# Kernel optimization log

Measured on AMD Instinct MI355X. Metric: run time of the kernel, lower is better.

The kernel has to match this reference:

```python
import math
import jax, jax.numpy as jnp
import numpy as np


def conv2d(x, w, b, pad=0, dil=1):
    # x: [B, Cin, H, W], w: [Cout, Cin, kh, kw] (OIHW)
    y = jax.lax.conv_general_dilated(
        x, w, window_strides=(1, 1),
        padding=[(pad, pad), (pad, pad)],
        rhs_dilation=(dil, dil),
        dimension_numbers=('NCHW', 'OIHW', 'NCHW'))
    return y + b[None, :, None, None]


def setup_inputs() -> dict:
    key = jax.random.key(0)
    ks = jax.random.split(key, 8)
    B, C, H, W = 2, 64, 96, 96
    inner = 64 // 18  # = 3, as in the torch module
    n_dil = 3
    s = 0.1
    x = jax.random.normal(ks[0], (B, C, H, W), jnp.float32)
    w_red = jax.random.normal(ks[1], (inner, C, 1, 1), jnp.float32) * s
    b_red = jax.random.normal(ks[2], (inner,), jnp.float32) * s
    w_dil = jax.random.normal(ks[3], (n_dil, inner, inner, 3, 3), jnp.float32) * s
    b_dil = jax.random.normal(ks[4], (n_dil, inner), jnp.float32) * s
    w_fuse = jax.random.normal(ks[5], (C, inner * n_dil * 6, 1, 1), jnp.float32) * s
    b_fuse = jax.random.normal(ks[6], (C,), jnp.float32) * s
    return {"x": x, "w_red": w_red, "b_red": b_red, "w_dil": w_dil,
            "b_dil": b_dil, "w_fuse": w_fuse, "b_fuse": b_fuse}


def _c4_transforms(x):
    # identity, flip-W, flip-H, rot90 k=1,2,3 over spatial dims
    return [x,
            jnp.flip(x, axis=-1),
            jnp.flip(x, axis=-2),
            jnp.rot90(x, 1, axes=(2, 3)),
            jnp.rot90(x, 2, axes=(2, 3)),
            jnp.rot90(x, 3, axes=(2, 3))]


def reference(x, w_red, b_red, w_dil, b_dil, w_fuse, b_fuse):
    dilations = (1, 2, 3)
    residual_scale = 0.2
    B, C, H, W = x.shape
    x_red = conv2d(x, w_red, b_red)                    # [B, inner, H, W]
    tfs = _c4_transforms(x_red)
    feats = []
    for i, d in enumerate(dilations):
        co = conv2d(x_red, w_dil[i], b_dil[i], pad=d, dil=d)
        for tf in tfs:
            feats.append(co * tf)
    cat = jnp.concatenate(feats, axis=1)               # [B, inner*18, H, W]
    fused = conv2d(cat, w_fuse, b_fuse)                # [B, C, H, W]
    tokens = fused.reshape(B, C, H * W).transpose(0, 2, 1)  # [B, N, C]
    # Chunked attention in the original is mathematically full self-attention
    scores = jnp.einsum('bnc,bmc->bnm', tokens, tokens) / math.sqrt(C)
    attn = jax.nn.softmax(scores, axis=-1)
    out = jnp.einsum('bnm,bmc->bnc', attn, tokens)     # [B, N, C]
    out = out.transpose(0, 2, 1).reshape(B, C, H, W)
    return x + residual_scale * out
```

## Files before the change

kernel.cpp:

```cpp
#include <hip/hip_runtime.h>

#define HW    96
#define NPIX  9216
#define NCH   64
#define INNER 3
#define NDIL  3
#define BB    2
#define TOTPIX (BB * NPIX)
#define NT32  (NPIX / 32)

typedef __attribute__((ext_vector_type(8))) short short8;
typedef __attribute__((ext_vector_type(8))) unsigned short ushort8;
typedef __attribute__((ext_vector_type(4))) float f32x4;
typedef __attribute__((ext_vector_type(4))) unsigned int uint32x4;

__device__ __forceinline__ ushort f2bf_rne(float f) {
    unsigned u = __float_as_uint(f);
    u += 0x7fffu + ((u >> 16) & 1u);
    return (ushort)(u >> 16);
}
__device__ __forceinline__ float bf2f(ushort u) {
    return __uint_as_float((unsigned)u << 16);
}
__device__ __forceinline__ unsigned pack_bf(float lo, float hi) {
    return __builtin_amdgcn_perm(__float_as_uint(hi), __float_as_uint(lo), 0x07060302u);
}

__global__ __launch_bounds__(256) void
k_reduce(const float* __restrict__ x, const float* __restrict__ w_red,
         const float* __restrict__ b_red, float* __restrict__ xred,
         float* __restrict__ L) {
    __shared__ float part[4][3][64];
    int tid = threadIdx.x;
    int gid = blockIdx.x * 256 + tid;
    if (gid < TOTPIX) L[gid] = 0.f;
    int cp = tid >> 6, lane = tid & 63;
    int pix = blockIdx.x * 64 + lane;
    int b = pix / NPIX, n = pix % NPIX;
    const float* xb = x + (size_t)b * NCH * NPIX + (size_t)(cp * 16) * NPIX + n;
    float a0 = 0.f, a1 = 0.f, a2 = 0.f;
    #pragma unroll
    for (int c = 0; c < 16; ++c) {
        float xv = xb[(size_t)c * NPIX];
        a0 = fmaf(w_red[0 * NCH + cp * 16 + c], xv, a0);
        a1 = fmaf(w_red[1 * NCH + cp * 16 + c], xv, a1);
        a2 = fmaf(w_red[2 * NCH + cp * 16 + c], xv, a2);
    }
    part[cp][0][lane] = a0; part[cp][1][lane] = a1; part[cp][2][lane] = a2;
    __syncthreads();
    if (tid < 192) {
        int o = tid >> 6, lp = tid & 63;
        float s = ((part[0][o][lp] + part[1][o][lp]) +
                   (part[2][o][lp] + part[3][o][lp])) + b_red[o];
        int pix2 = blockIdx.x * 64 + lp;
        int b2 = pix2 / NPIX, n2 = pix2 % NPIX;
        xred[((size_t)b2 * INNER + o) * NPIX + n2] = s;
    }
}

__global__ __launch_bounds__(256) void
k_featfuse(const float* __restrict__ xred, const float* __restrict__ w_dil,
           const float* __restrict__ b_dil, const float* __restrict__ w_fuse,
           const float* __restrict__ b_fuse, ushort* __restrict__ tok,
           ushort* __restrict__ tokTt) {
    __shared__ ushort wpad[64 * 72];
    __shared__ float  bsh[64];
    __shared__ ushort FTt[64 * 70];
    __shared__ ushort tile[64 * 72];

    int tid = threadIdx.x;
    for (int i = tid; i < 64 * 64; i += 256) {
        int c = i >> 6, j = i & 63;
        wpad[c * 72 + j] = (j < 54) ? f2bf_rne(w_fuse[c * 54 + j]) : (ushort)0;
    }
    if (tid < 64) bsh[tid] = b_fuse[tid];

    int px0 = blockIdx.x * 64;

    if (tid < 192) {
        int lp = tid & 63, i3 = tid >> 6;
        int pix = px0 + lp;
        int b = pix / NPIX, n = pix % NPIX;
        int h = n / HW, w = n % HW;
        const float* xr = xred + (size_t)b * INNER * NPIX;
        int d = i3 + 1;

        float co[3] = {b_dil[i3 * 3 + 0], b_dil[i3 * 3 + 1], b_dil[i3 * 3 + 2]};
        #pragma unroll
        for (int ci = 0; ci < 3; ++ci) {
            const float* xo = xr + ci * NPIX;
            #pragma unroll
            for (int kh = 0; kh < 3; ++kh) {
                int hh = h + (kh - 1) * d;
                #pragma unroll
                for (int kw = 0; kw < 3; ++kw) {
                    int ww = w + (kw - 1) * d;
                    float v = ((unsigned)hh < HW && (unsigned)ww < HW)
                                  ? xo[hh * HW + ww] : 0.f;
                    #pragma unroll
                    for (int o = 0; o < 3; ++o)
                        co[o] = fmaf(w_dil[(9 * i3 + 3 * o + ci) * 9 + kh * 3 + kw],
                                     v, co[o]);
                }
            }
        }

        float tf[6][3];
        #pragma unroll
        for (int o = 0; o < 3; ++o) {
            const float* xo = xr + o * NPIX;
            tf[0][o] = xo[h * HW + w];
            tf[1][o] = xo[h * HW + (HW - 1 - w)];
            tf[2][o] = xo[(HW - 1 - h) * HW + w];
            tf[3][o] = xo[w * HW + (HW - 1 - h)];
            tf[4][o] = xo[(HW - 1 - h) * HW + (HW - 1 - w)];
            tf[5][o] = xo[(HW - 1 - w) * HW + h];
        }

        #pragma unroll
        for (int t = 0; t < 6; ++t)
            #pragma unroll
            for (int o = 0; o < 3; ++o)
                FTt[(i3 * 18 + t * 3 + o) * 70 + lp] = f2bf_rne(co[o] * tf[t][o]);
    } else {
        for (int i = tid - 192; i < 640; i += 64)
            FTt[(54 + (i >> 6)) * 70 + (i & 63)] = (ushort)0;
    }
    __syncthreads();

    int wv = tid >> 6, lane = tid & 63, quad = lane >> 4, l15 = lane & 15;

    short8 af[4][2];
    #pragma unroll
    for (int m = 0; m < 4; ++m)
        #pragma unroll
        for (int kc = 0; kc < 2; ++kc)
            af[m][kc] = *(const short8*)&wpad[(16 * m + l15) * 72 + quad * 8 + 32 * kc];

    f32x4 acc[4];
    #pragma unroll
    for (int m = 0; m < 4; ++m) acc[m] = (f32x4){0.f, 0.f, 0.f, 0.f};

    int pxl = wv * 16 + l15;
    #pragma unroll
    for (int kc = 0; kc < 2; ++kc) {
        short8 bf;
        #pragma unroll
        for (int jj = 0; jj < 8; ++jj)
            bf[jj] = (short)FTt[(quad * 8 + jj + 32 * kc) * 70 + pxl];
        #pragma unroll
        for (int m = 0; m < 4; ++m)
            acc[m] = __builtin_amdgcn_mfma_f32_16x16x32_bf16(af[m][kc], bf, acc[m], 0, 0, 0);
    }

    #pragma unroll
    for (int m = 0; m < 4; ++m)
        #pragma unroll
        for (int r = 0; r < 4; ++r) {
            int c = 16 * m + quad * 4 + r;
            tile[c * 72 + wv * 16 + l15] = f2bf_rne(acc[m][r] + bsh[c]);
        }
    __syncthreads();

    int b0 = px0 / NPIX, n0 = px0 % NPIX;
    {
        int lp = tid >> 2, part = tid & 3;
        ushort row[16];
        #pragma unroll
        for (int k = 0; k < 16; ++k) row[k] = tile[(part * 16 + k) * 72 + lp];
        ushort* dst = tok + ((size_t)b0 * NPIX + n0 + lp) * NCH + part * 16;
        *(ushort8*)&dst[0] = *(const ushort8*)&row[0];
        *(ushort8*)&dst[8] = *(const ushort8*)&row[8];
    }
    {
        int c = tid >> 2, seg = tid & 3;
        int n = n0 + seg * 16;
        size_t base = (((size_t)b0 * NT32 + (n >> 5)) * 64 + c) * 32 + (n & 31);
        *(ushort8*)&tokTt[base]     = *(const ushort8*)&tile[c * 72 + seg * 16];
        *(ushort8*)&tokTt[base + 8] = *(const ushort8*)&tile[c * 72 + seg * 16 + 8];
    }
}

__global__ __launch_bounds__(256, 5) void
k_attn(const ushort* __restrict__ tok, const ushort* __restrict__ tokTt,
       float* __restrict__ L, ushort* __restrict__ pacc, int P, int KP) {
    __shared__ ushort smem[9728];
    ushort* ldsK = smem;
    ushort* ldsV = smem + 4608;

    const int QW = NPIX / 128;
    int bid0 = blockIdx.x;
    int nwg = gridDim.x;
    int bid = (bid0 & 7) * (nwg >> 3) + (bid0 >> 3);
    int qc = bid % QW; int rest = bid / QW;
    int p = rest % P;  int b = rest / P;
    int tid = threadIdx.x;
    int wv = tid >> 6, lane = tid & 63;
    int quad = lane >> 4, l15 = lane & 15;

    const ushort* tb  = tok + (size_t)b * NPIX * NCH;
    const ushort* tvb = tokTt + (size_t)b * NT32 * (64 * 32);
    int qwave = qc * 128 + wv * 32;

    int sk_off = (tid >> 3) * 72 + (tid & 7) * 8;
    int svj = tid & 3;
    int sv_b0 = (tid >> 2) * 40 + 8 * ((2 * svj) & 3) + 4 * (svj >> 1);
    int sv_b1 = (tid >> 2) * 40 + 8 * ((2 * svj + 1) & 3) + 4 * (svj >> 1);

    short8 qf[2][2];
    const float scale = 0.125f * 1.44269504088896340736f;
    #pragma unroll
    for (int n = 0; n < 2; ++n) {
        const ushort* qr = tb + (size_t)(qwave + 16 * n + l15) * NCH + quad * 8;
        #pragma unroll
        for (int kc = 0; kc < 2; ++kc) {
            ushort8 raw = *(const ushort8*)(qr + 32 * kc);
            short8 f;
            #pragma unroll
            for (int e = 0; e < 8; ++e) f[e] = (short)f2bf_rne(bf2f(raw[e]) * scale);
            qf[n][kc] = f;
        }
    }

    f32x4 O[4][2];
    #pragma unroll
    for (int m = 0; m < 4; ++m)
        #pragma unroll
        for (int n = 0; n < 2; ++n) O[m][n] = (f32x4){0.f, 0.f, 0.f, 0.f};
    float lrun[2] = {0.f, 0.f};

    const float FM = 16.0f;
    const f32x4 FMc = (f32x4){-FM, -FM, -FM, -FM};

    int k0 = p * KP;
    int nt = KP / 32;

    const ushort* pK = tb + (size_t)k0 * NCH + tid * 8;
    const ushort* pV = tvb + ((size_t)(k0 >> 5)) * 2048 + tid * 8;

    {
        ushort8 gK = *(const ushort8*)pK;
        ushort8 gV = *(const ushort8*)pV;
        *(ushort8*)&ldsK[sk_off] = gK;
        uint32x4 v4 = *(uint32x4*)&gV;
        *(uint2*)&ldsV[sv_b0] = make_uint2(v4.x, v4.y);
        *(uint2*)&ldsV[sv_b1] = make_uint2(v4.z, v4.w);
    }
    __syncthreads();

    for (int t = 0; t < nt; ++t) {
        int curK = (t & 1) * 2304, curV = (t & 1) * 2560;
        bool pre = (t + 1 < nt);
        pK += 32 * NCH;  pV += 2048;

        ushort8 nK, nV;
        if (pre) {
            nK = *(const ushort8*)pK;
            nV = *(const ushort8*)pV;
        }

        short8 kd[4];
        #pragma unroll
        for (int m2 = 0; m2 < 2; ++m2)
            #pragma unroll
            for (int kc = 0; kc < 2; ++kc)
                kd[2 * m2 + kc] = *(const short8*)&ldsK[curK + (16 * m2 + l15) * 72 +
                                                       quad * 8 + 32 * kc];

        uint32x4 wac[2];
        #pragma unroll
        for (int m2 = 0; m2 < 2; ++m2) {
            f32x4 Sm[2];
            __builtin_amdgcn_s_setprio(1);
            #pragma unroll
            for (int n = 0; n < 2; ++n) {
                Sm[n] = __builtin_amdgcn_mfma_f32_16x16x32_bf16(kd[2 * m2 + 0],
                                                                qf[n][0], FMc, 0, 0, 0);
                Sm[n] = __builtin_amdgcn_mfma_f32_16x16x32_bf16(kd[2 * m2 + 1],
                                                                qf[n][1], Sm[n], 0, 0, 0);
            }
            __builtin_amdgcn_s_setprio(0);
            #pragma unroll
            for (int n = 0; n < 2; ++n) {
                float e0 = __builtin_amdgcn_exp2f(Sm[n][0]);
                float e1 = __builtin_amdgcn_exp2f(Sm[n][1]);
                float e2 = __builtin_amdgcn_exp2f(Sm[n][2]);
                float e3 = __builtin_amdgcn_exp2f(Sm[n][3]);
                lrun[n] += (e0 + e1) + (e2 + e3);
                if (m2 == 0) {
                    wac[n].x = pack_bf(e0, e1); wac[n].y = pack_bf(e2, e3);
                } else {
                    wac[n].z = pack_bf(e0, e1); wac[n].w = pack_bf(e2, e3);
                }
            }
        }

        if (pre) {
            *(ushort8*)&ldsK[(curK ^ 2304) + sk_off] = nK;
            uint32x4 v4 = *(uint32x4*)&nV;
            *(uint2*)&ldsV[(curV ^ 2560) + sv_b0] = make_uint2(v4.x, v4.y);
            *(uint2*)&ldsV[(curV ^ 2560) + sv_b1] = make_uint2(v4.z, v4.w);
        }

        short8 vf[4];
        #pragma unroll
        for (int mc = 0; mc < 4; ++mc)
            vf[mc] = *(const short8*)&ldsV[curV + (16 * mc + l15) * 40 + quad * 8];

        __builtin_amdgcn_s_setprio(1);
        #pragma unroll
        for (int n = 0; n < 2; ++n) {
            short8 bfr = *(short8*)&wac[n];
            #pragma unroll
            for (int mc = 0; mc < 4; ++mc)
                O[mc][n] = __builtin_amdgcn_mfma_f32_16x16x32_bf16(vf[mc], bfr,
                                                                   O[mc][n], 0, 0, 0);
        }
        __builtin_amdgcn_s_setprio(0);

        __syncthreads();
    }

    #pragma unroll
    for (int n = 0; n < 2; ++n) {
        lrun[n] += __shfl_xor(lrun[n], 16, 64);
        lrun[n] += __shfl_xor(lrun[n], 32, 64);
    }
    if (quad == 0) {
        #pragma unroll
        for (int n = 0; n < 2; ++n)
            atomicAdd(&L[(size_t)b * NPIX + qwave + 16 * n + l15], lrun[n]);
    }

    #pragma unroll
    for (int n = 0; n < 2; ++n) {
        int ql = wv * 32 + 16 * n + l15;
        #pragma unroll
        for (int m = 0; m < 4; ++m)
            #pragma unroll
            for (int r = 0; r < 4; ++r)
                smem[(16 * m + quad * 4 + r) * 136 + ql] = f2bf_rne(O[m][n][r]);
    }
    __syncthreads();
    size_t bp = (size_t)b * P + p;
    #pragma unroll
    for (int i = 0; i < 4; ++i) {
        int lin = i * 2048 + tid * 8;
        int c = lin >> 7, q = lin & 127;
        *(ushort8*)(pacc + (bp * NCH + c) * NPIX + qc * 128 + q) =
            *(const ushort8*)&smem[c * 136 + q];
    }
}

__global__ void k_combine(const float* __restrict__ x, const float* __restrict__ L,
                          const ushort* __restrict__ pacc, float* __restrict__ out,
                          int P) {
    int gid = blockIdx.x * blockDim.x + threadIdx.x;
    if (gid >= BB * NCH * (NPIX / 8)) return;
    int seg = gid % (NPIX / 8);
    int bc  = gid / (NPIX / 8);
    int b = bc / NCH;
    int n0 = seg * 8;
    float o[8] = {0.f, 0.f, 0.f, 0.f, 0.f, 0.f, 0.f, 0.f};
    for (int p = 0; p < P; ++p) {
        ushort8 t = *(const ushort8*)(pacc +
            (((size_t)b * P + p) * NCH + (bc % NCH)) * NPIX + n0);
        #pragma unroll
        for (int e = 0; e < 8; ++e) o[e] += bf2f(t[e]);
    }
    const float* lv = L + (size_t)b * NPIX + n0;
    const float* xb = x + (size_t)bc * NPIX + n0;
    float* ob = out + (size_t)bc * NPIX + n0;
    #pragma unroll
    for (int e = 0; e < 8; ++e)
        ob[e] = fmaf(0.2f / lv[e], o[e], xb[e]);
}

extern "C" void kernel_launch(void* const* d_in, const int* in_sizes, int n_in,
                              void* d_out, int out_size, void* d_ws, size_t ws_size,
                              hipStream_t stream) {
    const float* x      = (const float*)d_in[0];
    const float* w_red  = (const float*)d_in[1];
    const float* b_red  = (const float*)d_in[2];
    const float* w_dil  = (const float*)d_in[3];
    const float* b_dil  = (const float*)d_in[4];
    const float* w_fuse = (const float*)d_in[5];
    const float* b_fuse = (const float*)d_in[6];
    float* out = (float*)d_out;

    const size_t XRED_N = (size_t)BB * INNER * NPIX;
    const size_t TOK_N  = (size_t)BB * NPIX * NCH;
    const size_t HEAD_B = XRED_N * 4 + 2 * TOK_N * 2 + TOTPIX * 4;
    int P = 0;
    const int cands[4] = {8, 4, 2, 1};
    for (int ci = 0; ci < 4; ++ci) {
        int cp = cands[ci];
        size_t need = HEAD_B + (size_t)BB * cp * NPIX * NCH * 2;
        if (ws_size >= need) { P = cp; break; }
    }
    if (P == 0) return;

    float*  xred  = (float*)d_ws;
    ushort* tok   = (ushort*)(xred + XRED_N);
    ushort* tokTt = tok + TOK_N;
    float*  L     = (float*)(tokTt + TOK_N);
    ushort* pacc  = (ushort*)(L + TOTPIX);

    k_reduce  <<<TOTPIX / 64, 256, 0, stream>>>(x, w_red, b_red, xred, L);
    k_featfuse<<<TOTPIX / 64, 256, 0, stream>>>(xred, w_dil, b_dil, w_fuse,
                                                b_fuse, tok, tokTt);
    k_attn    <<<BB * P * (NPIX / 128), 256, 0, stream>>>(tok, tokTt, L, pacc,
                                                          P, NPIX / P);
    k_combine <<<(BB * NCH * (NPIX / 8) + 255) / 256, 256, 0, stream>>>(x, L, pacc,
                                                                        out, P);
}
```

Measured before the change: 137.8 us.

## Process two key tiles per barrier with doubled LDS double-buffering in attention

The attention loop now stages two 32-key K/V tiles per iteration into a double-buffered LDS region twice the size of before. It issues the global prefetches for both next tiles up front and runs the tile body twice between barriers, so the number of __syncthreads drops by half. The larger shared memory footprint lowers the occupancy hint from 5 to 4 blocks per CU, and more prefetch registers are live at once. It also assumes KP/32 is even.

```diff
diff --git a/kernel.cpp b/kernel.cpp
--- a/kernel.cpp
+++ b/kernel.cpp
@@ -181,12 +181,67 @@
     }
 }
 
-__global__ __launch_bounds__(256, 5) void
+__device__ __forceinline__ void
+attn_body(const ushort* __restrict__ Kb, const ushort* __restrict__ Vb,
+          int l15, int quad, const short8 (&qf)[2][2], f32x4 FMc,
+          f32x4 (&O)[4][2], float (&lrun)[2]) {
+    short8 kd[4];
+    #pragma unroll
+    for (int m2 = 0; m2 < 2; ++m2)
+        #pragma unroll
+        for (int kc = 0; kc < 2; ++kc)
+            kd[2 * m2 + kc] = *(const short8*)&Kb[(16 * m2 + l15) * 72 +
+                                                  quad * 8 + 32 * kc];
+
+    uint32x4 wac[2];
+    #pragma unroll
+    for (int m2 = 0; m2 < 2; ++m2) {
+        f32x4 Sm[2];
+        __builtin_amdgcn_s_setprio(1);
+        #pragma unroll
+        for (int n = 0; n < 2; ++n) {
+            Sm[n] = __builtin_amdgcn_mfma_f32_16x16x32_bf16(kd[2 * m2 + 0],
+                                                            qf[n][0], FMc, 0, 0, 0);
+            Sm[n] = __builtin_amdgcn_mfma_f32_16x16x32_bf16(kd[2 * m2 + 1],
+                                                            qf[n][1], Sm[n], 0, 0, 0);
+        }
+        __builtin_amdgcn_s_setprio(0);
+        #pragma unroll
+        for (int n = 0; n < 2; ++n) {
+            float e0 = __builtin_amdgcn_exp2f(Sm[n][0]);
+            float e1 = __builtin_amdgcn_exp2f(Sm[n][1]);
+            float e2 = __builtin_amdgcn_exp2f(Sm[n][2]);
+            float e3 = __builtin_amdgcn_exp2f(Sm[n][3]);
+            lrun[n] += (e0 + e1) + (e2 + e3);
+            if (m2 == 0) {
+                wac[n].x = pack_bf(e0, e1); wac[n].y = pack_bf(e2, e3);
+            } else {
+                wac[n].z = pack_bf(e0, e1); wac[n].w = pack_bf(e2, e3);
+            }
+        }
+    }
+
+    short8 vf[4];
+    #pragma unroll
+    for (int mc = 0; mc < 4; ++mc)
+        vf[mc] = *(const short8*)&Vb[(16 * mc + l15) * 40 + quad * 8];
+
+    __builtin_amdgcn_s_setprio(1);
+    #pragma unroll
+    for (int n = 0; n < 2; ++n) {
+        short8 bfr = *(short8*)&wac[n];
+        #pragma unroll
+        for (int mc = 0; mc < 4; ++mc)
+            O[mc][n] = __builtin_amdgcn_mfma_f32_16x16x32_bf16(vf[mc], bfr,
+                                                               O[mc][n], 0, 0, 0);
+    }
+    __builtin_amdgcn_s_setprio(0);
+}
+
+__global__ __launch_bounds__(256, 4) void
 k_attn(const ushort* __restrict__ tok, const ushort* __restrict__ tokTt,
        float* __restrict__ L, ushort* __restrict__ pacc, int P, int KP) {
-    __shared__ ushort smem[9728];
-    ushort* ldsK = smem;
-    ushort* ldsV = smem + 4608;
+    __shared__ ushort smem[19456];
 
     const int QW = NPIX / 128;
     int bid0 = blockIdx.x;
@@ -233,90 +288,58 @@
     const f32x4 FMc = (f32x4){-FM, -FM, -FM, -FM};
 
     int k0 = p * KP;
-    int nt = KP / 32;
+    int nw = (KP / 32) >> 1;
 
     const ushort* pK = tb + (size_t)k0 * NCH + tid * 8;
     const ushort* pV = tvb + ((size_t)(k0 >> 5)) * 2048 + tid * 8;
 
     {
-        ushort8 gK = *(const ushort8*)pK;
-        ushort8 gV = *(const ushort8*)pV;
-        *(ushort8*)&ldsK[sk_off] = gK;
-        uint32x4 v4 = *(uint32x4*)&gV;
-        *(uint2*)&ldsV[sv_b0] = make_uint2(v4.x, v4.y);
-        *(uint2*)&ldsV[sv_b1] = make_uint2(v4.z, v4.w);
-    }
+        ushort8 gK0 = *(const ushort8*)pK;
+        ushort8 gK1 = *(const ushort8*)(pK + 32 * NCH);
+        ushort8 gV0 = *(const ushort8*)pV;
+        ushort8 gV1 = *(const ushort8*)(pV + 2048);
+        *(ushort8*)&smem[sk_off] = gK0;
+        *(ushort8*)&smem[2304 + sk_off] = gK1;
+        uint32x4 v4 = *(uint32x4*)&gV0;
+        *(uint2*)&smem[4608 + sv_b0] = make_uint2(v4.x, v4.y);
+        *(uint2*)&smem[4608 + sv_b1] = make_uint2(v4.z, v4.w);
+        v4 = *(uint32x4*)&gV1;
+        *(uint2*)&smem[7168 + sv_b0] = make_uint2(v4.x, v4.y);
+        *(uint2*)&smem[7168 + sv_b1] = make_uint2(v4.z, v4.w);
+    }
+    pK += 64 * NCH;  pV += 4096;
     __syncthreads();
 
-    for (int t = 0; t < nt; ++t) {
-        int curK = (t & 1) * 2304, curV = (t & 1) * 2560;
-        bool pre = (t + 1 < nt);
-        pK += 32 * NCH;  pV += 2048;
-
-        ushort8 nK, nV;
+    for (int w = 0; w < nw; ++w) {
+        int base  = (w & 1) * 9728;
+        int obase = base ^ 9728;
+        bool pre = (w + 1 < nw);
+
+        ushort8 nK0, nK1, nV0, nV1;
         if (pre) {
-            nK = *(const ushort8*)pK;
-            nV = *(const ushort8*)pV;
-        }
-
-        short8 kd[4];
-        #pragma unroll
-        for (int m2 = 0; m2 < 2; ++m2)
-            #pragma unroll
-            for (int kc = 0; kc < 2; ++kc)
-                kd[2 * m2 + kc] = *(const short8*)&ldsK[curK + (16 * m2 + l15) * 72 +
-                                                       quad * 8 + 32 * kc];
-
-        uint32x4 wac[2];
-        #pragma unroll
-        for (int m2 = 0; m2 < 2; ++m2) {
-            f32x4 Sm[2];
-            __builtin_amdgcn_s_setprio(1);
-            #pragma unroll
-            for (int n = 0; n < 2; ++n) {
-                Sm[n] = __builtin_amdgcn_mfma_f32_16x16x32_bf16(kd[2 * m2 + 0],
-                                                                qf[n][0], FMc, 0, 0, 0);
-                Sm[n] = __builtin_amdgcn_mfma_f32_16x16x32_bf16(kd[2 * m2 + 1],
-                                                                qf[n][1], Sm[n], 0, 0, 0);
-            }
-            __builtin_amdgcn_s_setprio(0);
-            #pragma unroll
-            for (int n = 0; n < 2; ++n) {
-                float e0 = __builtin_amdgcn_exp2f(Sm[n][0]);
-                float e1 = __builtin_amdgcn_exp2f(Sm[n][1]);
-                float e2 = __builtin_amdgcn_exp2f(Sm[n][2]);
-                float e3 = __builtin_amdgcn_exp2f(Sm[n][3]);
-                lrun[n] += (e0 + e1) + (e2 + e3);
-                if (m2 == 0) {
-                    wac[n].x = pack_bf(e0, e1); wac[n].y = pack_bf(e2, e3);
-                } else {
-                    wac[n].z = pack_bf(e0, e1); wac[n].w = pack_bf(e2, e3);
-                }
-            }
-        }
-
+            nK0 = *(const ushort8*)pK;
+            nV0 = *(const ushort8*)pV;
+            nK1 = *(const ushort8*)(pK + 32 * NCH);
+            nV1 = *(const ushort8*)(pV + 2048);
+            pK += 64 * NCH;  pV += 4096;
+        }
+
+        attn_body(&smem[base], &smem[base + 4608], l15, quad, qf, FMc, O, lrun);
         if (pre) {
-            *(ushort8*)&ldsK[(curK ^ 2304) + sk_off] = nK;
-            uint32x4 v4 = *(uint32x4*)&nV;
-            *(uint2*)&ldsV[(curV ^ 2560) + sv_b0] = make_uint2(v4.x, v4.y);
-            *(uint2*)&ldsV[(curV ^ 2560) + sv_b1] = make_uint2(v4.z, v4.w);
-        }
-
-        short8 vf[4];
-        #pragma unroll
-        for (int mc = 0; mc < 4; ++mc)
-            vf[mc] = *(const short8*)&ldsV[curV + (16 * mc + l15) * 40 + quad * 8];
-
-        __builtin_amdgcn_s_setprio(1);
-        #pragma unroll
-        for (int n = 0; n < 2; ++n) {
-            short8 bfr = *(short8*)&wac[n];
-            #pragma unroll
-            for (int mc = 0; mc < 4; ++mc)
-                O[mc][n] = __builtin_amdgcn_mfma_f32_16x16x32_bf16(vf[mc], bfr,
-                                                                   O[mc][n], 0, 0, 0);
-        }
-        __builtin_amdgcn_s_setprio(0);
+            *(ushort8*)&smem[obase + sk_off] = nK0;
+            uint32x4 v4 = *(uint32x4*)&nV0;
+            *(uint2*)&smem[obase + 4608 + sv_b0] = make_uint2(v4.x, v4.y);
+            *(uint2*)&smem[obase + 4608 + sv_b1] = make_uint2(v4.z, v4.w);
+        }
+
+        attn_body(&smem[base + 2304], &smem[base + 7168], l15, quad, qf, FMc,
+                  O, lrun);
+        if (pre) {
+            *(ushort8*)&smem[obase + 2304 + sk_off] = nK1;
+            uint32x4 v4 = *(uint32x4*)&nV1;
+            *(uint2*)&smem[obase + 7168 + sv_b0] = make_uint2(v4.x, v4.y);
+            *(uint2*)&smem[obase + 7168 + sv_b1] = make_uint2(v4.z, v4.w);
+        }
 
         __syncthreads();
     }
```

Result: slower. 142.8 us (+3.6%).
